# Performance work log

Hardware: AMD Instinct MI355X
Metric: run time of the kernel (lower is better)

The kernel has to match this reference:

```python
import jax, jax.numpy as jnp
import numpy as np

NUM_GROUPS = 32
EPS = 1e-6


def group_norm(x, gamma, beta):
    # x: [B, C, H, W]; GroupNorm over (C//G, H, W) per group, affine per-channel
    B, C, H, W = x.shape
    xg = x.reshape(B, NUM_GROUPS, C // NUM_GROUPS, H, W)
    mean = xg.mean(axis=(2, 3, 4), keepdims=True)
    var = ((xg - mean) ** 2).mean(axis=(2, 3, 4), keepdims=True)
    xg = (xg - mean) * jax.lax.rsqrt(var + EPS)
    x = xg.reshape(B, C, H, W)
    return x * gamma[None, :, None, None] + beta[None, :, None, None]


def setup_inputs() -> dict:
    key = jax.random.key(0)
    ks = jax.random.split(key, 8)
    n, t, c, h, w = 2, 16, 64, 64, 64
    M = 512  # memory-bank slots
    inv_sqrt_c = 1.0 / np.sqrt(c).astype(np.float32)
    return {
        "x": jax.random.normal(ks[0], (n, t, c, h, w), jnp.float32),
        "gn_gamma": 1.0 + 0.1 * jax.random.normal(ks[1], (c,), jnp.float32),
        "gn_beta": 0.1 * jax.random.normal(ks[2], (c,), jnp.float32),
        "phi_w": jax.random.normal(ks[3], (c, c), jnp.float32) * inv_sqrt_c,
        "phi_b": 0.01 * jax.random.normal(ks[4], (c,), jnp.float32),
        "mb": jax.random.normal(ks[5], (c, M), jnp.float32),
        "wz_w": jax.random.normal(ks[6], (c, c), jnp.float32) * inv_sqrt_c,
        "wz_b": 0.01 * jax.random.normal(ks[7], (c,), jnp.float32),
    }


def reference(x, gn_gamma, gn_beta, phi_w, phi_b, mb, wz_w, wz_b):
    # Faithful MMA forward, batched across all t frames at once (the torch
    # code loops per-frame; math is identical frame-wise).
    n, t, c, h, w = x.shape
    xb = x.reshape(n * t, c, h, w)
    q_ = group_norm(xb, gn_gamma, gn_beta)
    # 1x1 conv == per-pixel channel matmul
    phi = jnp.einsum('oc,bchw->bohw', phi_w, q_) + phi_b[None, :, None, None]
    phi = phi.reshape(n * t, c, h * w).transpose(0, 2, 1)  # [B, HW, C]
    scale = jnp.asarray(c, phi.dtype) ** -0.5
    f1 = jnp.einsum('bpc,cm->bpm', phi, mb) * scale          # [B, HW, 512]
    attn = jax.nn.softmax(f1, axis=-1)
    y1 = jnp.einsum('bpm,cm->bpc', attn, mb)                 # [B, HW, C]
    y1 = y1.transpose(0, 2, 1).reshape(n * t, c, h, w)
    wy = jnp.einsum('oc,bchw->bohw', wz_w, y1) + wz_b[None, :, None, None]
    out = wy + xb  # residual with the (pre-norm) frame, as in torch
    return out.reshape(n, t, c, h, w)
```

## Files before the change

kernel.cpp:

```cpp
#include <hip/hip_runtime.h>
#include <hip/hip_bf16.h>

#define NFRAME 32
#define CCH 64
#define HW 4096
#define MSLOT 512

typedef __attribute__((ext_vector_type(8))) short s16x8;
typedef __attribute__((ext_vector_type(16))) float f32x16;
typedef __attribute__((ext_vector_type(4))) unsigned int u32x4;
typedef __attribute__((ext_vector_type(2))) unsigned int u32x2;
typedef unsigned short u16;
typedef unsigned int u32;

#define WS_STATS 0
#define WS_OFF   2048
#define WS_BF16  4096
#define BW_KV    0
#define BW_WZF   65536
#define BW_WFF   69632

#define QSCALE 0.18033688011112042f

static __device__ __forceinline__ u16 f2b(float f) {
  __hip_bfloat16 h = __float2bfloat16(f);
  return *reinterpret_cast<u16*>(&h);
}
static __device__ __forceinline__ u32 pack2(float a, float b) {
  u32 r;
  asm("v_cvt_pk_bf16_f32 %0, %1, %2" : "=v"(r) : "v"(a), "v"(b));
  return r;
}
static __device__ __forceinline__ f32x16 zero16() {
  f32x16 z;
#pragma unroll
  for (int r = 0; r < 16; ++r) z[r] = 0.f;
  return z;
}
static __device__ __forceinline__ void d2b(const float* e, s16x8& f0, s16x8& f1) {
#pragma unroll
  for (int mh = 0; mh < 2; ++mh) {
    const u32 P0 = pack2(e[mh * 8 + 0], e[mh * 8 + 1]);
    const u32 P1 = pack2(e[mh * 8 + 2], e[mh * 8 + 3]);
    const u32 Q0 = pack2(e[mh * 8 + 4], e[mh * 8 + 5]);
    const u32 Q1 = pack2(e[mh * 8 + 6], e[mh * 8 + 7]);
    const u32x2 s0 = __builtin_amdgcn_permlane32_swap(P0, Q0, false, false);
    const u32x2 s1 = __builtin_amdgcn_permlane32_swap(P1, Q1, false, false);
    u32x4 bw = {s0[0], s1[0], s0[1], s1[1]};
    if (mh == 0) f0 = __builtin_bit_cast(s16x8, bw);
    else         f1 = __builtin_bit_cast(s16x8, bw);
  }
}

__global__ __launch_bounds__(256) void k_pre(const float* __restrict__ x,
                                             const float* __restrict__ mb,
                                             const float* __restrict__ wz_w,
                                             float* __restrict__ ws) {
  if (blockIdx.x < 1024) {
    const int bg = blockIdx.x;
    const float4* xp = (const float4*)(x + (size_t)bg * 8192);
    const int t = threadIdx.x;
    float s = 0.f, s2 = 0.f;
#pragma unroll
    for (int i = 0; i < 8; ++i) {
      float4 v = xp[t + i * 256];
      s  += v.x + v.y + v.z + v.w;
      s2 += v.x * v.x + v.y * v.y + v.z * v.z + v.w * v.w;
    }
    for (int off = 32; off; off >>= 1) {
      s  += __shfl_down(s,  off, 64);
      s2 += __shfl_down(s2, off, 64);
    }
    __shared__ float ls[8];
    const int wid = t >> 6;
    if ((t & 63) == 0) { ls[wid * 2] = s; ls[wid * 2 + 1] = s2; }
    __syncthreads();
    if (t == 0) {
      float S = 0.f, S2 = 0.f;
#pragma unroll
      for (int w = 0; w < 4; ++w) { S += ls[w * 2]; S2 += ls[w * 2 + 1]; }
      float mean = S * (1.f / 8192.f);
      float var  = S2 * (1.f / 8192.f) - mean * mean;
      float rstd = rsqrtf(var + 1e-6f);
      ws[WS_STATS + bg * 2]     = mean;
      ws[WS_STATS + bg * 2 + 1] = rstd;
    }
    return;
  }
  u16* wbw = (u16*)(ws + WS_BF16);
  const int i = (blockIdx.x - 1024) * 256 + threadIdx.x;
  if (i < 65536) {
    const int j = i & 7, l = (i >> 3) & 63, f = (i >> 9) & 7, mt = i >> 12;
    float v;
    if (f < 4) {
      const int c = f * 16 + ((l >> 5) << 3) + j;
      const int m = mt * 32 + (l & 31);
      v = mb[c * MSLOT + m];
    } else {
      const int idx = f - 4;
      const int c = (idx & 1) * 32 + (l & 31);
      const int m = mt * 32 + (idx >> 1) * 16 + ((l >> 5) << 3) + j;
      v = mb[c * MSLOT + m];
    }
    wbw[BW_KV + i] = f2b(v);
  } else {
    const int i3 = i - 65536;
    const int j = i3 & 7, l = (i3 >> 3) & 63, ks = (i3 >> 9) & 3, ot = i3 >> 11;
    const int o = ot * 32 + (l & 31);
    const int c = ks * 16 + ((l >> 5) << 3) + j;
    wbw[BW_WZF + i3] = f2b(wz_w[o * 64 + c]);
  }
}

__global__ __launch_bounds__(256) void k_prep(const float* __restrict__ phi_w,
                                              const float* __restrict__ phi_b,
                                              const float* __restrict__ gamma,
                                              const float* __restrict__ beta,
                                              float* __restrict__ ws) {
  const int b = blockIdx.x;
  const int o = threadIdx.x & 63;
  const int quad = threadIdx.x >> 6;
  __shared__ u16 wrow[64 * 64];
  __shared__ float offp[256];
  float offacc = 0.f;
#pragma unroll
  for (int ci = 0; ci < 16; ++ci) {
    const int c = quad * 16 + ci;
    const int g = c >> 1;
    const float mean = ws[WS_STATS + (b * 32 + g) * 2];
    const float rstd = ws[WS_STATS + (b * 32 + g) * 2 + 1];
    const float a = gamma[c] * rstd;
    const float d = beta[c] - mean * a;
    const float wv = phi_w[o * 64 + c];
    wrow[o * 64 + c] = f2b(wv * a * QSCALE);
    offacc += wv * d;
  }
  offp[threadIdx.x] = offacc;
  __syncthreads();
  if (quad == 0) {
    const float off = offp[o] + offp[64 + o] + offp[128 + o] + offp[192 + o];
    ws[WS_OFF + b * 64 + o] = (off + phi_b[o]) * QSCALE;
  }
  u16* wff = (u16*)(ws + WS_BF16) + BW_WFF + (size_t)b * 4096;
#pragma unroll
  for (int k = 0; k < 16; ++k) {
    const int il = threadIdx.x * 16 + k;
    const int j = il & 7, l = (il >> 3) & 63, ks = (il >> 9) & 3, ot = il >> 11;
    const int oo = ot * 32 + (l & 31);
    const int c = ks * 16 + ((l >> 5) << 3) + j;
    wff[il] = wrow[oo * 64 + c];
  }
}

__global__ __launch_bounds__(256, 4) void k_main(const float* __restrict__ x,
                                                 const float* __restrict__ ws,
                                                 const float* __restrict__ wz_b,
                                                 float* __restrict__ out) {
  const int b    = blockIdx.x >> 5;
  const int tile = blockIdx.x & 31;
  const int w    = threadIdx.x >> 6;
  const int lane = threadIdx.x & 63;
  const int l5 = lane & 31;
  const int hi = lane >> 5;
  const int p  = tile * 128 + w * 32 + l5;

  const u16* wb = (const u16*)(ws + WS_BF16);
  const float* xb = x + (size_t)b * CCH * HW;

  __shared__ __align__(16) u16 kv[2][8][512];

#define STAGE(mt_, nb_)                                                          \
  {                                                                              \
    _Pragma("unroll")                                                            \
    for (int k = 0; k < 2; ++k) {                                                \
      const int f = w * 2 + k;                                                   \
      const u16* src = wb + BW_KV + ((size_t)(mt_) * 8 + f) * 512 + lane * 8;    \
      __builtin_amdgcn_global_load_lds(                                          \
          (const __attribute__((address_space(1))) void*)src,                    \
          (__attribute__((address_space(3))) void*)&kv[nb_][f][0], 16, 0, 0);    \
    }                                                                            \
  }

  STAGE(0, 0);

  s16x8 q[4];
  {
    s16x8 bx[4];
#pragma unroll
    for (int ks = 0; ks < 4; ++ks) {
      const float* xc = xb + (size_t)(ks * 16 + hi * 8) * HW + p;
      float v[8];
#pragma unroll
      for (int j = 0; j < 8; ++j) v[j] = xc[(size_t)j * HW];
      u32x4 pk = {pack2(v[0], v[1]), pack2(v[2], v[3]),
                  pack2(v[4], v[5]), pack2(v[6], v[7])};
      bx[ks] = __builtin_bit_cast(s16x8, pk);
    }
    const float* offb = ws + WS_OFF + b * 64;
#pragma unroll
    for (int ot = 0; ot < 2; ++ot) {
      f32x16 acc = zero16();
#pragma unroll
      for (int ks = 0; ks < 4; ++ks) {
        const s16x8 a = *(const s16x8*)(wb + BW_WFF + ((((size_t)b * 2 + ot) * 4 + ks) * 64 + lane) * 8);
        acc = __builtin_amdgcn_mfma_f32_32x32x16_bf16(a, bx[ks], acc, 0, 0, 0);
      }
      float e[16];
#pragma unroll
      for (int rq = 0; rq < 4; ++rq) {
        const float4 offv = *(const float4*)(offb + ot * 32 + rq * 8 + hi * 4);
#pragma unroll
        for (int rr = 0; rr < 4; ++rr) e[rq * 4 + rr] = acc[rq * 4 + rr] + ((const float*)&offv)[rr];
      }
      d2b(e, q[ot * 2], q[ot * 2 + 1]);
    }
  }

  f32x16 Y[2];
#pragma unroll
  for (int ct = 0; ct < 2; ++ct) Y[ct] = zero16();
  float Lacc = 0.f;

  __syncthreads();

#pragma unroll 2
  for (int mt = 0; mt < 16; ++mt) {
    const int cb = mt & 1;

    s16x8 kf[4], vf[4];
#pragma unroll
    for (int ks = 0; ks < 4; ++ks)
      kf[ks] = *(const s16x8*)&kv[cb][ks][(size_t)lane * 8];
#pragma unroll
    for (int i = 0; i < 4; ++i)
      vf[i] = *(const s16x8*)&kv[cb][4 + i][(size_t)lane * 8];

    if (mt < 15) STAGE(mt + 1, cb ^ 1);

    f32x16 s = zero16();
#pragma unroll
    for (int ks = 0; ks < 4; ++ks)
      s = __builtin_amdgcn_mfma_f32_32x32x16_bf16(kf[ks], q[ks], s, 0, 0, 0);
    float e[16];
    float ls = 0.f;
#pragma unroll
    for (int r = 0; r < 16; ++r) { e[r] = exp2f(s[r]); ls += e[r]; }
    Lacc += ls;
    s16x8 pf0, pf1;
    d2b(e, pf0, pf1);
#pragma unroll
    for (int ct = 0; ct < 2; ++ct) {
      Y[ct] = __builtin_amdgcn_mfma_f32_32x32x16_bf16(vf[ct],     pf0, Y[ct], 0, 0, 0);
      Y[ct] = __builtin_amdgcn_mfma_f32_32x32x16_bf16(vf[2 + ct], pf1, Y[ct], 0, 0, 0);
    }
    __syncthreads();
  }

  const float Ltot = Lacc + __shfl_xor(Lacc, 32, 64);
  const float invL = 1.f / Ltot;

  s16x8 by[4];
#pragma unroll
  for (int ct = 0; ct < 2; ++ct) {
    float e[16];
#pragma unroll
    for (int r = 0; r < 16; ++r) e[r] = Y[ct][r] * invL;
    d2b(e, by[ct * 2], by[ct * 2 + 1]);
  }

  const float* xr = xb + p;
  float* ob = out + (size_t)b * CCH * HW + p;
#pragma unroll
  for (int ot = 0; ot < 2; ++ot) {
    f32x16 acc = zero16();
#pragma unroll
    for (int ks = 0; ks < 4; ++ks) {
      const s16x8 a = *(const s16x8*)(wb + BW_WZF + (((size_t)ot * 4 + ks) * 64 + lane) * 8);
      acc = __builtin_amdgcn_mfma_f32_32x32x16_bf16(a, by[ks], acc, 0, 0, 0);
    }
#pragma unroll
    for (int rq = 0; rq < 4; ++rq) {
      const int obase = ot * 32 + rq * 8 + hi * 4;
      const float4 bz = *(const float4*)(wz_b + obase);
#pragma unroll
      for (int rr = 0; rr < 4; ++rr) {
        const size_t idx = (size_t)(obase + rr) * HW;
        ob[idx] = acc[rq * 4 + rr] + ((const float*)&bz)[rr] + xr[idx];
      }
    }
  }
#undef STAGE
}

extern "C" void kernel_launch(void* const* d_in, const int* in_sizes, int n_in,
                              void* d_out, int out_size, void* d_ws, size_t ws_size,
                              hipStream_t stream) {
  const float* x     = (const float*)d_in[0];
  const float* gamma = (const float*)d_in[1];
  const float* beta  = (const float*)d_in[2];
  const float* phi_w = (const float*)d_in[3];
  const float* phi_b = (const float*)d_in[4];
  const float* mb    = (const float*)d_in[5];
  const float* wz_w  = (const float*)d_in[6];
  const float* wz_b  = (const float*)d_in[7];
  float* out = (float*)d_out;
  float* ws  = (float*)d_ws;

  k_pre<<<1296, 256, 0, stream>>>(x, mb, wz_w, ws);
  k_prep<<<32, 256, 0, stream>>>(phi_w, phi_b, gamma, beta, ws);
  k_main<<<NFRAME * 32, 256, 0, stream>>>(x, ws, wz_b, out);
}
```

Before: 48.86 us.

## Triple-buffer K/V LDS tiles and prefetch next K fragments into registers

Moves the LDS ring for memory-bank K/V tiles from two stages to three, so global-to-LDS loads are issued two iterations ahead. It also ping-pongs K fragment registers, loading the next tile's K from LDS during the softmax/exp phase before the PV MFMAs, and fully unrolls the loop. The aim is to hide global load latency and LDS read latency behind MFMA and exp work. In exchange it uses more LDS and more registers, which could affect occupancy at launch_bounds(256,4).

```diff
diff --git a/kernel.cpp b/kernel.cpp
--- a/kernel.cpp
+++ b/kernel.cpp
@@ -167,7 +167,7 @@
   const u16* wb = (const u16*)(ws + WS_BF16);
   const float* xb = x + (size_t)b * CCH * HW;
 
-  __shared__ __align__(16) u16 kv[2][8][512];
+  __shared__ __align__(16) u16 kv[3][8][512];
 
 #define STAGE(mt_, nb_)                                                          \
   {                                                                              \
@@ -182,6 +182,7 @@
   }
 
   STAGE(0, 0);
+  STAGE(1, 1);
 
   s16x8 q[4];
   {
@@ -223,38 +224,49 @@
 
   __syncthreads();
 
-#pragma unroll 2
-  for (int mt = 0; mt < 16; ++mt) {
-    const int cb = mt & 1;
-
-    s16x8 kf[4], vf[4];
-#pragma unroll
-    for (int ks = 0; ks < 4; ++ks)
-      kf[ks] = *(const s16x8*)&kv[cb][ks][(size_t)lane * 8];
-#pragma unroll
-    for (int i = 0; i < 4; ++i)
-      vf[i] = *(const s16x8*)&kv[cb][4 + i][(size_t)lane * 8];
-
-    if (mt < 15) STAGE(mt + 1, cb ^ 1);
-
-    f32x16 s = zero16();
-#pragma unroll
-    for (int ks = 0; ks < 4; ++ks)
-      s = __builtin_amdgcn_mfma_f32_32x32x16_bf16(kf[ks], q[ks], s, 0, 0, 0);
-    float e[16];
-    float ls = 0.f;
-#pragma unroll
-    for (int r = 0; r < 16; ++r) { e[r] = exp2f(s[r]); ls += e[r]; }
-    Lacc += ls;
-    s16x8 pf0, pf1;
-    d2b(e, pf0, pf1);
-#pragma unroll
-    for (int ct = 0; ct < 2; ++ct) {
-      Y[ct] = __builtin_amdgcn_mfma_f32_32x32x16_bf16(vf[ct],     pf0, Y[ct], 0, 0, 0);
-      Y[ct] = __builtin_amdgcn_mfma_f32_32x32x16_bf16(vf[2 + ct], pf1, Y[ct], 0, 0, 0);
-    }
-    __syncthreads();
-  }
+  s16x8 kfA[4], kfB[4];
+#pragma unroll
+  for (int ks = 0; ks < 4; ++ks)
+    kfA[ks] = *(const s16x8*)&kv[0][ks][(size_t)lane * 8];
+
+#define BODY(mt_, KFC, KFN)                                                      \
+  {                                                                              \
+    const int cb = (mt_) % 3;                                                    \
+    s16x8 vf[4];                                                                 \
+    _Pragma("unroll")                                                            \
+    for (int i = 0; i < 4; ++i)                                                  \
+      vf[i] = *(const s16x8*)&kv[cb][4 + i][(size_t)lane * 8];                   \
+    if ((mt_) <= 13) STAGE((mt_) + 2, ((mt_) + 2) % 3);                          \
+    f32x16 s = zero16();                                                         \
+    _Pragma("unroll")                                                            \
+    for (int ks = 0; ks < 4; ++ks)                                               \
+      s = __builtin_amdgcn_mfma_f32_32x32x16_bf16(KFC[ks], q[ks], s, 0, 0, 0);   \
+    float e[16];                                                                 \
+    float ls = 0.f;                                                              \
+    _Pragma("unroll")                                                            \
+    for (int r = 0; r < 16; ++r) { e[r] = exp2f(s[r]); ls += e[r]; }             \
+    Lacc += ls;                                                                  \
+    s16x8 pf0, pf1;                                                              \
+    d2b(e, pf0, pf1);                                                            \
+    if ((mt_) < 15) {                                                            \
+      const int nb = ((mt_) + 1) % 3;                                            \
+      _Pragma("unroll")                                                          \
+      for (int ks = 0; ks < 4; ++ks)                                             \
+        KFN[ks] = *(const s16x8*)&kv[nb][ks][(size_t)lane * 8];                  \
+    }                                                                            \
+    Y[0] = __builtin_amdgcn_mfma_f32_32x32x16_bf16(vf[0], pf0, Y[0], 0, 0, 0);   \
+    Y[1] = __builtin_amdgcn_mfma_f32_32x32x16_bf16(vf[1], pf0, Y[1], 0, 0, 0);   \
+    Y[0] = __builtin_amdgcn_mfma_f32_32x32x16_bf16(vf[2], pf1, Y[0], 0, 0, 0);   \
+    Y[1] = __builtin_amdgcn_mfma_f32_32x32x16_bf16(vf[3], pf1, Y[1], 0, 0, 0);   \
+    __syncthreads();                                                             \
+  }
+
+#pragma unroll
+  for (int mt2 = 0; mt2 < 8; ++mt2) {
+    BODY(2 * mt2,     kfA, kfB);
+    BODY(2 * mt2 + 1, kfB, kfA);
+  }
+#undef BODY
 
   const float Ltot = Lacc + __shfl_xor(Lacc, 32, 64);
   const float invL = 1.f / Ltot;
```

Measured after the change: 179.7 us. 268% more time.

## Use 512-thread blocks and stage KV bank in two large halves

Applied to the files above, without the earlier changes.

Doubles k_main block size to 8 waves covering 256 pixels, halving the grid. The memory bank is no longer double-buffered per 32-slot tile with a barrier every iteration. Each half (256 slots) is loaded into a 64KB LDS buffer with only two barrier points in total. This cuts per-iteration synchronisation and amortizes KV loading over more pixels. The cost is that the second-half load is not overlapped with compute, and the larger LDS footprint may lower occupancy.

```diff
diff --git a/kernel.cpp b/kernel.cpp
--- a/kernel.cpp
+++ b/kernel.cpp
@@ -152,36 +152,36 @@
   }
 }
 
-__global__ __launch_bounds__(256, 4) void k_main(const float* __restrict__ x,
+__global__ __launch_bounds__(512, 4) void k_main(const float* __restrict__ x,
                                                  const float* __restrict__ ws,
                                                  const float* __restrict__ wz_b,
                                                  float* __restrict__ out) {
-  const int b    = blockIdx.x >> 5;
-  const int tile = blockIdx.x & 31;
+  const int b    = blockIdx.x >> 4;
+  const int tile = blockIdx.x & 15;
   const int w    = threadIdx.x >> 6;
   const int lane = threadIdx.x & 63;
   const int l5 = lane & 31;
   const int hi = lane >> 5;
-  const int p  = tile * 128 + w * 32 + l5;
+  const int p  = tile * 256 + w * 32 + l5;
 
   const u16* wb = (const u16*)(ws + WS_BF16);
   const float* xb = x + (size_t)b * CCH * HW;
 
-  __shared__ __align__(16) u16 kv[2][8][512];
-
-#define STAGE(mt_, nb_)                                                          \
+  __shared__ __align__(16) u16 kv[8][8][512];
+
+#define STAGEH(h_)                                                               \
   {                                                                              \
     _Pragma("unroll")                                                            \
-    for (int k = 0; k < 2; ++k) {                                                \
-      const int f = w * 2 + k;                                                   \
-      const u16* src = wb + BW_KV + ((size_t)(mt_) * 8 + f) * 512 + lane * 8;    \
+    for (int r = 0; r < 8; ++r) {                                                \
+      const u16* src = wb + BW_KV + ((size_t)(((h_) * 8 + r) * 8 + w)) * 512     \
+                       + lane * 8;                                               \
       __builtin_amdgcn_global_load_lds(                                          \
           (const __attribute__((address_space(1))) void*)src,                    \
-          (__attribute__((address_space(3))) void*)&kv[nb_][f][0], 16, 0, 0);    \
+          (__attribute__((address_space(3))) void*)&kv[r][w][0], 16, 0, 0);      \
     }                                                                            \
   }
 
-  STAGE(0, 0);
+  STAGEH(0);
 
   s16x8 q[4];
   {
@@ -224,19 +224,14 @@
   __syncthreads();
 
 #pragma unroll 2
-  for (int mt = 0; mt < 16; ++mt) {
-    const int cb = mt & 1;
-
+  for (int mt = 0; mt < 8; ++mt) {
     s16x8 kf[4], vf[4];
 #pragma unroll
     for (int ks = 0; ks < 4; ++ks)
-      kf[ks] = *(const s16x8*)&kv[cb][ks][(size_t)lane * 8];
+      kf[ks] = *(const s16x8*)&kv[mt][ks][(size_t)lane * 8];
 #pragma unroll
     for (int i = 0; i < 4; ++i)
-      vf[i] = *(const s16x8*)&kv[cb][4 + i][(size_t)lane * 8];
-
-    if (mt < 15) STAGE(mt + 1, cb ^ 1);
-
+      vf[i] = *(const s16x8*)&kv[mt][4 + i][(size_t)lane * 8];
     f32x16 s = zero16();
 #pragma unroll
     for (int ks = 0; ks < 4; ++ks)
@@ -248,12 +243,40 @@
     Lacc += ls;
     s16x8 pf0, pf1;
     d2b(e, pf0, pf1);
-#pragma unroll
-    for (int ct = 0; ct < 2; ++ct) {
-      Y[ct] = __builtin_amdgcn_mfma_f32_32x32x16_bf16(vf[ct],     pf0, Y[ct], 0, 0, 0);
-      Y[ct] = __builtin_amdgcn_mfma_f32_32x32x16_bf16(vf[2 + ct], pf1, Y[ct], 0, 0, 0);
-    }
-    __syncthreads();
+    Y[0] = __builtin_amdgcn_mfma_f32_32x32x16_bf16(vf[0], pf0, Y[0], 0, 0, 0);
+    Y[1] = __builtin_amdgcn_mfma_f32_32x32x16_bf16(vf[1], pf0, Y[1], 0, 0, 0);
+    Y[0] = __builtin_amdgcn_mfma_f32_32x32x16_bf16(vf[2], pf1, Y[0], 0, 0, 0);
+    Y[1] = __builtin_amdgcn_mfma_f32_32x32x16_bf16(vf[3], pf1, Y[1], 0, 0, 0);
+  }
+
+  __syncthreads();
+  STAGEH(1);
+  __syncthreads();
+
+#pragma unroll 2
+  for (int mt = 0; mt < 8; ++mt) {
+    s16x8 kf[4], vf[4];
+#pragma unroll
+    for (int ks = 0; ks < 4; ++ks)
+      kf[ks] = *(const s16x8*)&kv[mt][ks][(size_t)lane * 8];
+#pragma unroll
+    for (int i = 0; i < 4; ++i)
+      vf[i] = *(const s16x8*)&kv[mt][4 + i][(size_t)lane * 8];
+    f32x16 s = zero16();
+#pragma unroll
+    for (int ks = 0; ks < 4; ++ks)
+      s = __builtin_amdgcn_mfma_f32_32x32x16_bf16(kf[ks], q[ks], s, 0, 0, 0);
+    float e[16];
+    float ls = 0.f;
+#pragma unroll
+    for (int r = 0; r < 16; ++r) { e[r] = exp2f(s[r]); ls += e[r]; }
+    Lacc += ls;
+    s16x8 pf0, pf1;
+    d2b(e, pf0, pf1);
+    Y[0] = __builtin_amdgcn_mfma_f32_32x32x16_bf16(vf[0], pf0, Y[0], 0, 0, 0);
+    Y[1] = __builtin_amdgcn_mfma_f32_32x32x16_bf16(vf[1], pf0, Y[1], 0, 0, 0);
+    Y[0] = __builtin_amdgcn_mfma_f32_32x32x16_bf16(vf[2], pf1, Y[0], 0, 0, 0);
+    Y[1] = __builtin_amdgcn_mfma_f32_32x32x16_bf16(vf[3], pf1, Y[1], 0, 0, 0);
   }
 
   const float Ltot = Lacc + __shfl_xor(Lacc, 32, 64);
@@ -289,7 +312,7 @@
       }
     }
   }
-#undef STAGE
+#undef STAGEH
 }
 
 extern "C" void kernel_launch(void* const* d_in, const int* in_sizes, int n_in,
@@ -308,5 +331,5 @@
 
   k_pre<<<1296, 256, 0, stream>>>(x, mb, wz_w, ws);
   k_prep<<<32, 256, 0, stream>>>(phi_w, phi_b, gamma, beta, ws);
-  k_main<<<NFRAME * 32, 256, 0, stream>>>(x, ws, wz_b, out);
-}
+  k_main<<<NFRAME * 16, 512, 0, stream>>>(x, ws, wz_b, out);
+}
```

Result: faster. 46.87 us, median of 2 (-4.1%).
